# Kernel optimization log

Measured on AMD Instinct MI355X. Metric: run time of the kernel, lower is better.

## Reference

```python
import jax, jax.numpy as jnp
import numpy as np
from jax import lax

H = 24  # hidden_states
FORGET_BIAS = 1.0  # TF LSTMCell default


def setup_inputs() -> dict:
    key = jax.random.key(0)
    ks = jax.random.split(key, 10)
    B, T, V, E, C = 256, 512, 50000, 200, 3
    return {
        "words": jax.random.randint(ks[0], (B, T), 0, V, dtype=jnp.int32),
        "capitals": jax.random.randint(ks[1], (B, T), 0, C, dtype=jnp.int32),
        "Ew": jax.random.normal(ks[2], (V, E), dtype=jnp.float32),
        "Ec": jax.random.normal(ks[3], (C, C), dtype=jnp.float32),
        "W_lstm": jax.random.normal(ks[4], (E + C + H, 4 * H), dtype=jnp.float32) * 0.1,
        "b_lstm": jnp.zeros((4 * H,), dtype=jnp.float32),
        "W1": jax.random.normal(ks[5], (H, 50), dtype=jnp.float32) * 0.2,
        "b1": jnp.full((50,), 0.1, dtype=jnp.float32),
        "W2": jax.random.normal(ks[6], (50, 6), dtype=jnp.float32) * 0.2,
        "b2": jnp.zeros((6,), dtype=jnp.float32),
    }


def reference(words, capitals, Ew, Ec, W_lstm, b_lstm, W1, b1, W2, b2):
    # embed + concat: [B, T, 203]
    x = jnp.concatenate([Ew[words], Ec[capitals]], axis=-1)
    B = x.shape[0]
    xs = jnp.swapaxes(x, 0, 1)  # [T, B, F]

    def step(carry, xt):
        c, h = carry
        z = jnp.concatenate([xt, h], axis=-1) @ W_lstm + b_lstm  # [B, 4H]
        i, j, f, o = jnp.split(z, 4, axis=-1)  # TF gate order i, j, f, o
        c = jax.nn.sigmoid(f + FORGET_BIAS) * c + jax.nn.sigmoid(i) * jnp.tanh(j)
        h = jax.nn.sigmoid(o) * jnp.tanh(c)
        return (c, h), h

    init = (jnp.zeros((B, H), x.dtype), jnp.zeros((B, H), x.dtype))
    _, hs = lax.scan(step, init, xs)  # hs: [T, B, H]

    last = hs.mean(axis=0)                       # mean-pool over time: [B, H]
    layer = jax.nn.elu(last @ W1 + b1)           # [B, 50]
    return jax.nn.sigmoid(layer @ W2 + b2)       # [B, 6]
```

## Files before the change

### kernel.cpp

```cpp
#include <hip/hip_runtime.h>

typedef float f2 __attribute__((ext_vector_type(2)));

constexpr int Tt = 512;
constexpr int Bb = 256;
constexpr int Ee = 200;
constexpr int Gg = 96;
constexpr int Vv = 50000;

__device__ __forceinline__ float fast_rcp(float x) { return __builtin_amdgcn_rcpf(x); }
__device__ __forceinline__ float sigf(float x) { return fast_rcp(1.f + __expf(-x)); }
__device__ __forceinline__ float tanhf_(float x) {
    float e = __expf(2.f * x);
    return 1.f - 2.f * fast_rcp(e + 1.f);
}

__global__ __launch_bounds__(256) void ew_proj(const float* __restrict__ Ew,
                                               const float* __restrict__ Wl,
                                               float* __restrict__ EwW)
{
    constexpr int BM = 32, BK = 8;
    __shared__ float As[BK][BM];
    __shared__ float Bs[BK][Gg];
    const int tid = threadIdx.x;
    const int w0  = blockIdx.x * BM;
    const int tc  = tid & 15;
    const int tr  = tid >> 4;
    float acc0[6] = {0.f, 0.f, 0.f, 0.f, 0.f, 0.f};
    float acc1[6] = {0.f, 0.f, 0.f, 0.f, 0.f, 0.f};

    for (int k0 = 0; k0 < Ee; k0 += BK) {
        {
            const int kk = tid & 7;
            const int m  = tid >> 3;
            const int w  = w0 + m;
            As[kk][m] = (w < Vv) ? Ew[w * Ee + k0 + kk] : 0.f;
        }
        {
            const int kk = tid >> 5;
            const int gb = (tid & 31) * 3;
            #pragma unroll
            for (int u = 0; u < 3; ++u) {
                const int g  = gb + u;
                const int gp = (g % 24) * 4 + (g / 24);
                Bs[kk][gp] = Wl[(k0 + kk) * Gg + g];
            }
        }
        __syncthreads();
        #pragma unroll
        for (int kk = 0; kk < BK; ++kk) {
            const float a0 = As[kk][tr * 2 + 0];
            const float a1 = As[kk][tr * 2 + 1];
            float bb[6];
            #pragma unroll
            for (int u = 0; u < 6; ++u) bb[u] = Bs[kk][tc * 6 + u];
            #pragma unroll
            for (int u = 0; u < 6; ++u) {
                acc0[u] += a0 * bb[u];
                acc1[u] += a1 * bb[u];
            }
        }
        __syncthreads();
    }
    const int wa = w0 + tr * 2;
    if (wa < Vv) {
        #pragma unroll
        for (int u = 0; u < 6; ++u) EwW[wa * Gg + tc * 6 + u] = acc0[u];
    }
    if (wa + 1 < Vv) {
        #pragma unroll
        for (int u = 0; u < 6; ++u) EwW[(wa + 1) * Gg + tc * 6 + u] = acc1[u];
    }
}

__global__ __launch_bounds__(64, 1) void lstm_head(
    const int* __restrict__ words, const int* __restrict__ caps,
    const float* __restrict__ Ec,  const float* __restrict__ Wl,
    const float* __restrict__ bl,  const float* __restrict__ EwW,
    const float* __restrict__ W1,  const float* __restrict__ b1,
    const float* __restrict__ W2,  const float* __restrict__ b2,
    float* __restrict__ out)
{
    __shared__ float4 EcB[3][24];
    __shared__ float4 hbuf4[2][6];
    __shared__ float  a1buf[2][50];

    const int  lane = threadIdx.x;
    const int  half = lane >> 5;
    const int  j    = lane & 31;
    const int  jc   = (j < 24) ? j : 23;
    const bool act  = (j < 24);
    const int  b    = blockIdx.x * 2 + half;

    for (int e = lane; e < 72; e += 64) {
        const int cap = e / 24, jj = e % 24;
        float4 v;
        #pragma unroll
        for (int c = 0; c < 4; ++c) {
            float s = bl[c * 24 + jj];
            #pragma unroll
            for (int kk = 0; kk < 3; ++kk)
                s += Ec[cap * 3 + kk] * Wl[(200 + kk) * Gg + c * 24 + jj];
            (&v.x)[c] = s;
        }
        EcB[cap][jj] = v;
    }
    if (act) ((float*)hbuf4)[half * 24 + jc] = 0.f;
    __syncthreads();

    f2 uij[24], ufo[24];
    #pragma unroll
    for (int k = 0; k < 24; ++k) {
        const int base = (203 + k) * Gg;
        f2 a, o2;
        a.x  = Wl[base + 0  + jc];
        a.y  = Wl[base + 24 + jc];
        o2.x = Wl[base + 48 + jc];
        o2.y = Wl[base + 72 + jc];
        uij[k] = a;
        ufo[k] = o2;
    }

    const int* wrow = words + b * Tt;
    const int* crow = caps  + b * Tt;
    const int  off  = jc * 4;

    int wi2 = wrow[2];
    int cp0 = crow[0], cp1 = crow[1], cp2 = crow[2];
    float4 x0 = *(const float4*)(EwW + (long)wrow[0] * Gg + off);
    float4 x1 = *(const float4*)(EwW + (long)wrow[1] * Gg + off);

    float cstate = 0.f, hsum = 0.f;

    for (int t = 0; t < Tt; ++t) {
        const float4 x2 = *(const float4*)(EwW + (long)wi2 * Gg + off);
        const int tn  = (t + 3 < Tt) ? (t + 3) : (Tt - 1);
        const int wi3 = wrow[tn];
        const int cp3 = crow[tn];

        const float4 ecb = EcB[cp0][jc];
        f2 zij, zfo;
        zij.x = x0.x + ecb.x;  zij.y = x0.y + ecb.y;
        zfo.x = x0.z + ecb.z;  zfo.y = x0.w + ecb.w;

        float4 hv[6];
        #pragma unroll
        for (int q = 0; q < 6; ++q) hv[q] = hbuf4[half][q];

        #pragma unroll
        for (int k = 0; k < 24; ++k) {
            const float hk = (&hv[k >> 2].x)[k & 3];
            f2 hk2; hk2.x = hk; hk2.y = hk;
            zij += hk2 * uij[k];
            zfo += hk2 * ufo[k];
        }

        const float ig = sigf(zij.x);
        const float tj = tanhf_(zij.y);
        const float fg = sigf(zfo.x + 1.0f);
        const float og = sigf(zfo.y);
        cstate = fg * cstate + ig * tj;
        const float hn = og * tanhf_(cstate);
        hsum += hn;
        if (act) ((float*)hbuf4)[half * 24 + jc] = hn;
        __syncthreads();

        x0 = x1; x1 = x2;
        wi2 = wi3;
        cp0 = cp1; cp1 = cp2; cp2 = cp3;
    }

    if (act) ((float*)hbuf4)[half * 24 + jc] = hsum * (1.f / (float)Tt);
    __syncthreads();

    float4 mv[6];
    #pragma unroll
    for (int q = 0; q < 6; ++q) mv[q] = hbuf4[half][q];

    if (j < 25) {
        #pragma unroll
        for (int p = 0; p < 2; ++p) {
            const int q = j + p * 25;
            float s = b1[q];
            #pragma unroll
            for (int k = 0; k < 24; ++k)
                s += (&mv[k >> 2].x)[k & 3] * W1[k * 50 + q];
            a1buf[half][q] = (s > 0.f) ? s : (__expf(s) - 1.f);
        }
    }
    __syncthreads();

    if (j < 6) {
        float s = b2[j];
        for (int q = 0; q < 50; ++q) s += a1buf[half][q] * W2[q * 6 + j];
        out[b * 6 + j] = sigf(s);
    }
}

extern "C" void kernel_launch(void* const* d_in, const int* in_sizes, int n_in,
                              void* d_out, int out_size, void* d_ws, size_t ws_size,
                              hipStream_t stream)
{
    const int*   words = (const int*)d_in[0];
    const int*   caps  = (const int*)d_in[1];
    const float* Ew    = (const float*)d_in[2];
    const float* Ec    = (const float*)d_in[3];
    const float* Wl    = (const float*)d_in[4];
    const float* bl    = (const float*)d_in[5];
    const float* W1    = (const float*)d_in[6];
    const float* b1    = (const float*)d_in[7];
    const float* W2    = (const float*)d_in[8];
    const float* b2    = (const float*)d_in[9];
    float* out = (float*)d_out;
    float* EwW = (float*)d_ws;

    ew_proj<<<(Vv + 31) / 32, 256, 0, stream>>>(Ew, Wl, EwW);
    lstm_head<<<Bb / 2, 64, 0, stream>>>(words, caps, Ec, Wl, bl, EwW,
                                         W1, b1, W2, b2, out);
}
```

Baseline: 329.8 us.

## Broadcast LSTM hidden state via ds_swizzle and widen projection GEMM tile

The recurrent loop no longer writes h to shared memory and calls __syncthreads every timestep. Instead, each lane fetches h_k from lane k of its 32-lane half with ds_swizzle, which takes the LDS round trip and barrier off the serial 512-step chain. The dot product is split into two accumulator chains, and the word-row prefetch is deepened, including the capital-bias lookup. Separately, the vocabulary projection GEMM now uses 64-row tiles with float2 loads and packed f2 FMAs, trading more registers per thread for more reuse.

```diff
diff --git a/kernel.cpp b/kernel.cpp
--- a/kernel.cpp
+++ b/kernel.cpp
@@ -19,59 +19,63 @@
                                                const float* __restrict__ Wl,
                                                float* __restrict__ EwW)
 {
-    constexpr int BM = 32, BK = 8;
-    __shared__ float As[BK][BM];
-    __shared__ float Bs[BK][Gg];
+    __shared__ float As[8][64];
+    __shared__ float Bs[8][96];
     const int tid = threadIdx.x;
-    const int w0  = blockIdx.x * BM;
+    const int w0  = blockIdx.x * 64;
+    const int tr  = tid >> 4;
     const int tc  = tid & 15;
-    const int tr  = tid >> 4;
-    float acc0[6] = {0.f, 0.f, 0.f, 0.f, 0.f, 0.f};
-    float acc1[6] = {0.f, 0.f, 0.f, 0.f, 0.f, 0.f};
-
-    for (int k0 = 0; k0 < Ee; k0 += BK) {
+    const int am  = tid >> 2;
+    const int ak  = (tid & 3) * 2;
+    const int bk  = tid >> 5;
+    const int bg  = (tid & 31) * 3;
+
+    f2 acc[4][3] = {};
+
+    for (int k0 = 0; k0 < Ee; k0 += 8) {
         {
-            const int kk = tid & 7;
-            const int m  = tid >> 3;
-            const int w  = w0 + m;
-            As[kk][m] = (w < Vv) ? Ew[w * Ee + k0 + kk] : 0.f;
-        }
-        {
-            const int kk = tid >> 5;
-            const int gb = (tid & 31) * 3;
-            #pragma unroll
-            for (int u = 0; u < 3; ++u) {
-                const int g  = gb + u;
-                const int gp = (g % 24) * 4 + (g / 24);
-                Bs[kk][gp] = Wl[(k0 + kk) * Gg + g];
+            const int w = w0 + am;
+            f2 av = {0.f, 0.f};
+            if (w < Vv) av = *(const f2*)(Ew + (long)w * Ee + k0 + ak);
+            As[ak][am]     = av.x;
+            As[ak + 1][am] = av.y;
+        }
+        #pragma unroll
+        for (int u = 0; u < 3; ++u) {
+            const int g  = bg + u;
+            const int gp = (g % 24) * 4 + (g / 24);
+            Bs[bk][gp] = Wl[(k0 + bk) * Gg + g];
+        }
+        __syncthreads();
+        #pragma unroll
+        for (int kk = 0; kk < 8; ++kk) {
+            const float4 a4 = *(const float4*)&As[kk][tr * 4];
+            f2 b[3];
+            #pragma unroll
+            for (int u = 0; u < 3; ++u) b[u] = *(const f2*)&Bs[kk][tc * 6 + u * 2];
+            #pragma unroll
+            for (int i = 0; i < 4; ++i) {
+                const float ai = (&a4.x)[i];
+                f2 a2 = {ai, ai};
+                #pragma unroll
+                for (int u = 0; u < 3; ++u) acc[i][u] += a2 * b[u];
             }
         }
         __syncthreads();
-        #pragma unroll
-        for (int kk = 0; kk < BK; ++kk) {
-            const float a0 = As[kk][tr * 2 + 0];
-            const float a1 = As[kk][tr * 2 + 1];
-            float bb[6];
-            #pragma unroll
-            for (int u = 0; u < 6; ++u) bb[u] = Bs[kk][tc * 6 + u];
-            #pragma unroll
-            for (int u = 0; u < 6; ++u) {
-                acc0[u] += a0 * bb[u];
-                acc1[u] += a1 * bb[u];
-            }
-        }
-        __syncthreads();
-    }
-    const int wa = w0 + tr * 2;
-    if (wa < Vv) {
-        #pragma unroll
-        for (int u = 0; u < 6; ++u) EwW[wa * Gg + tc * 6 + u] = acc0[u];
-    }
-    if (wa + 1 < Vv) {
-        #pragma unroll
-        for (int u = 0; u < 6; ++u) EwW[(wa + 1) * Gg + tc * 6 + u] = acc1[u];
-    }
-}
+    }
+    #pragma unroll
+    for (int i = 0; i < 4; ++i) {
+        const int w = w0 + tr * 4 + i;
+        if (w < Vv) {
+            #pragma unroll
+            for (int u = 0; u < 3; ++u)
+                *(f2*)(EwW + (long)w * Gg + tc * 6 + u * 2) = acc[i][u];
+        }
+    }
+}
+
+#define REP24(M) M(0)M(1)M(2)M(3)M(4)M(5)M(6)M(7)M(8)M(9)M(10)M(11) \
+                 M(12)M(13)M(14)M(15)M(16)M(17)M(18)M(19)M(20)M(21)M(22)M(23)
 
 __global__ __launch_bounds__(64, 1) void lstm_head(
     const int* __restrict__ words, const int* __restrict__ caps,
@@ -82,7 +86,7 @@
     float* __restrict__ out)
 {
     __shared__ float4 EcB[3][24];
-    __shared__ float4 hbuf4[2][6];
+    __shared__ float  hmean[2][24];
     __shared__ float  a1buf[2][50];
 
     const int  lane = threadIdx.x;
@@ -105,77 +109,77 @@
         }
         EcB[cap][jj] = v;
     }
-    if (act) ((float*)hbuf4)[half * 24 + jc] = 0.f;
     __syncthreads();
 
-    f2 uij[24], ufo[24];
-    #pragma unroll
-    for (int k = 0; k < 24; ++k) {
-        const int base = (203 + k) * Gg;
-        f2 a, o2;
-        a.x  = Wl[base + 0  + jc];
-        a.y  = Wl[base + 24 + jc];
-        o2.x = Wl[base + 48 + jc];
-        o2.y = Wl[base + 72 + jc];
-        uij[k] = a;
-        ufo[k] = o2;
-    }
+#define DECL_U(K) f2 uij##K, ufo##K;
+    REP24(DECL_U)
+#undef DECL_U
+#define LOAD_U(K) { const int base_ = (203 + K) * Gg + jc;      \
+                    uij##K.x = Wl[base_ +  0];                  \
+                    uij##K.y = Wl[base_ + 24];                  \
+                    ufo##K.x = Wl[base_ + 48];                  \
+                    ufo##K.y = Wl[base_ + 72]; }
+    REP24(LOAD_U)
+#undef LOAD_U
 
     const int* wrow = words + b * Tt;
     const int* crow = caps  + b * Tt;
     const int  off  = jc * 4;
 
-    int wi2 = wrow[2];
-    int cp0 = crow[0], cp1 = crow[1], cp2 = crow[2];
     float4 x0 = *(const float4*)(EwW + (long)wrow[0] * Gg + off);
     float4 x1 = *(const float4*)(EwW + (long)wrow[1] * Gg + off);
-
-    float cstate = 0.f, hsum = 0.f;
+    float4 x2 = *(const float4*)(EwW + (long)wrow[2] * Gg + off);
+    int wi3 = wrow[3], wi4 = wrow[4];
+    int cp0 = crow[0], cp1 = crow[1], cp2 = crow[2], cp3 = crow[3], cp4 = crow[4];
+
+    float4 ecb = EcB[cp0][jc];
+    float cstate = 0.f, hsum = 0.f, hn = 0.f;
 
     for (int t = 0; t < Tt; ++t) {
-        const float4 x2 = *(const float4*)(EwW + (long)wi2 * Gg + off);
-        const int tn  = (t + 3 < Tt) ? (t + 3) : (Tt - 1);
-        const int wi3 = wrow[tn];
-        const int cp3 = crow[tn];
-
-        const float4 ecb = EcB[cp0][jc];
-        f2 zij, zfo;
-        zij.x = x0.x + ecb.x;  zij.y = x0.y + ecb.y;
-        zfo.x = x0.z + ecb.z;  zfo.y = x0.w + ecb.w;
-
-        float4 hv[6];
-        #pragma unroll
-        for (int q = 0; q < 6; ++q) hv[q] = hbuf4[half][q];
-
-        #pragma unroll
-        for (int k = 0; k < 24; ++k) {
-            const float hk = (&hv[k >> 2].x)[k & 3];
-            f2 hk2; hk2.x = hk; hk2.y = hk;
-            zij += hk2 * uij[k];
-            zfo += hk2 * ufo[k];
-        }
+        const float4 x3 = *(const float4*)(EwW + (long)wi3 * Gg + off);
+        const int tn  = (t + 5 < Tt) ? (t + 5) : (Tt - 1);
+        const int win = wrow[tn];
+        const int cpn = crow[tn];
+
+        f2 zij_a, zfo_a, zij_b = {0.f, 0.f}, zfo_b = {0.f, 0.f};
+        zij_a.x = x0.x + ecb.x;  zij_a.y = x0.y + ecb.y;
+        zfo_a.x = x0.z + ecb.z;  zfo_a.y = x0.w + ecb.w;
+
+        const int hu = __float_as_int(hn);
+#define STEP_A(K) { const float hk_ = __int_as_float(                          \
+                        __builtin_amdgcn_ds_swizzle(hu, ((K) << 5)));          \
+                    f2 h2_ = {hk_, hk_};                                       \
+                    zij_a += h2_ * uij##K;  zfo_a += h2_ * ufo##K; }
+#define STEP_B(K) { const float hk_ = __int_as_float(                          \
+                        __builtin_amdgcn_ds_swizzle(hu, ((K) << 5)));          \
+                    f2 h2_ = {hk_, hk_};                                       \
+                    zij_b += h2_ * uij##K;  zfo_b += h2_ * ufo##K; }
+        STEP_A(0)  STEP_A(1)  STEP_A(2)  STEP_A(3)  STEP_A(4)  STEP_A(5)
+        STEP_A(6)  STEP_A(7)  STEP_A(8)  STEP_A(9)  STEP_A(10) STEP_A(11)
+        STEP_B(12) STEP_B(13) STEP_B(14) STEP_B(15) STEP_B(16) STEP_B(17)
+        STEP_B(18) STEP_B(19) STEP_B(20) STEP_B(21) STEP_B(22) STEP_B(23)
+#undef STEP_A
+#undef STEP_B
+
+        const f2 zij = zij_a + zij_b;
+        const f2 zfo = zfo_a + zfo_b;
 
         const float ig = sigf(zij.x);
         const float tj = tanhf_(zij.y);
         const float fg = sigf(zfo.x + 1.0f);
         const float og = sigf(zfo.y);
         cstate = fg * cstate + ig * tj;
-        const float hn = og * tanhf_(cstate);
+        hn = og * tanhf_(cstate);
         hsum += hn;
-        if (act) ((float*)hbuf4)[half * 24 + jc] = hn;
-        __syncthreads();
-
-        x0 = x1; x1 = x2;
-        wi2 = wi3;
-        cp0 = cp1; cp1 = cp2; cp2 = cp3;
-    }
-
-    if (act) ((float*)hbuf4)[half * 24 + jc] = hsum * (1.f / (float)Tt);
+
+        ecb = EcB[cp1][jc];
+        x0 = x1; x1 = x2; x2 = x3;
+        wi3 = wi4; wi4 = win;
+        cp0 = cp1; cp1 = cp2; cp2 = cp3; cp3 = cp4; cp4 = cpn;
+    }
+
+    if (act) hmean[half][jc] = hsum * (1.f / (float)Tt);
     __syncthreads();
-
-    float4 mv[6];
-    #pragma unroll
-    for (int q = 0; q < 6; ++q) mv[q] = hbuf4[half][q];
 
     if (j < 25) {
         #pragma unroll
@@ -184,7 +188,7 @@
             float s = b1[q];
             #pragma unroll
             for (int k = 0; k < 24; ++k)
-                s += (&mv[k >> 2].x)[k & 3] * W1[k * 50 + q];
+                s += hmean[half][k] * W1[k * 50 + q];
             a1buf[half][q] = (s > 0.f) ? s : (__expf(s) - 1.f);
         }
     }
@@ -214,7 +218,7 @@
     float* out = (float*)d_out;
     float* EwW = (float*)d_ws;
 
-    ew_proj<<<(Vv + 31) / 32, 256, 0, stream>>>(Ew, Wl, EwW);
+    ew_proj<<<(Vv + 63) / 64, 256, 0, stream>>>(Ew, Wl, EwW);
     lstm_head<<<Bb / 2, 64, 0, stream>>>(words, caps, Ec, Wl, bl, EwW,
                                          W1, b1, W2, b2, out);
 }
```

Result: slower. 407.0 us (+23.4%).
